# Performance work log

Measured on AMD Instinct MI355X. Metric: run time of the kernel, lower is better.

The kernel has to match this reference:

```python
import jax, jax.numpy as jnp
import numpy as np

NUM_POINTS = 50
PMAX = 4096  # static per-ROI capacity (>> expected max ROI size ~2.2k)
EPS = 1e-5


def _bn(x, g, b):
    # BatchNorm1d in training mode: biased batch variance, eps=1e-5
    m = jnp.mean(x, axis=0)
    v = jnp.var(x, axis=0)
    return g * (x - m) * jax.lax.rsqrt(v + EPS) + b


def _fps(coords, valid, k):
    # coords: [P,3], valid: [P] bool. Classic PointNet++ FPS: start at idx 0,
    # iteratively pick argmax of running min squared distance. Invalid slots
    # pinned to -1 so they are never selected (while any valid point exists).
    dist0 = jnp.where(valid, 1e10, -1.0)

    def step(carry, _):
        dist, last = carry
        d = jnp.sum((coords - coords[last]) ** 2, axis=-1)
        dist = jnp.minimum(dist, jnp.where(valid, d, -1.0))
        nxt = jnp.argmax(dist).astype(jnp.int32)
        return (dist, nxt), nxt

    (_, _), rest = jax.lax.scan(step, (dist0, jnp.int32(0)), None, length=k - 1)
    return jnp.concatenate([jnp.zeros((1,), jnp.int32), rest])


def setup_inputs() -> dict:
    key = jax.random.key(0)
    ks = jax.random.split(key, 16)
    N, R, F, K = 500000, 256, 90, NUM_POINTS
    mid0, mid1, out_dim = 512, 256, 512

    def lin(k, i, o):
        return jax.random.normal(k, (i, o), jnp.float32) * 0.02, jnp.zeros((o,), jnp.float32)

    w1, b1 = lin(ks[0], F * K, mid1)
    w2, b2 = lin(ks[1], mid1, mid1)
    w3, b3 = lin(ks[2], mid1, mid0)
    w4, b4 = lin(ks[3], mid0, mid1)
    w5, b5 = lin(ks[4], mid1, out_dim)
    ones = lambda d: jnp.ones((d,), jnp.float32)
    zeros = lambda d: jnp.zeros((d,), jnp.float32)
    return {
        "cur_roi_nums": R,
        "cur_point_rois_idx": jax.random.randint(ks[5], (N,), 0, R, jnp.int32),
        "cur_points_features": jax.random.normal(ks[6], (N, F), jnp.float32),
        "cur_points_coords": jax.random.normal(ks[7], (N, 3), jnp.float32),
        "w1": w1, "b1": b1, "g1": ones(mid1), "be1": zeros(mid1),
        "w2": w2, "b2": b2, "g2": ones(mid1), "be2": zeros(mid1),
        "w3": w3, "b3": b3, "g3": ones(mid0), "be3": zeros(mid0),
        "w4": w4, "b4": b4, "g4": ones(mid1), "be4": zeros(mid1),
        "w5": w5, "b5": b5, "g5": ones(out_dim), "be5": zeros(out_dim),
    }


def reference(cur_roi_nums, cur_point_rois_idx, cur_points_features, cur_points_coords,
              w1, b1, g1, be1, w2, b2, g2, be2, w3, b3, g3, be3,
              w4, b4, g4, be4, w5, b5, g5, be5):
    R = int(cur_roi_nums)
    N = cur_points_coords.shape[0]
    idx = cur_point_rois_idx
    # Stable sort groups each ROI's points contiguously, preserving point order
    # (same order as the boolean-mask gather in the original loop).
    order = jnp.argsort(idx)
    counts = jnp.bincount(idx, length=R)            # [R]
    offsets = jnp.cumsum(counts) - counts            # [R]
    j = jnp.arange(PMAX)
    pos = offsets[:, None] + j[None, :]              # [R, PMAX]
    valid = j[None, :] < jnp.minimum(counts, PMAX)[:, None]
    gidx = jnp.take(order, jnp.clip(pos, 0, N - 1))  # [R, PMAX] global point ids
    coords_p = jnp.take(cur_points_coords, gidx, axis=0)  # [R, PMAX, 3]

    samp = jax.vmap(lambda c, v: _fps(c, v, NUM_POINTS))(coords_p, valid)  # [R, K]
    sg = jnp.take_along_axis(gidx, samp, axis=1)     # [R, K]
    feat = jnp.take(cur_points_features, sg, axis=0)  # [R, K, 90]
    feat = jnp.where((counts > 0)[:, None, None], feat, 0.0).reshape(R, -1)

    h = jax.nn.relu(_bn(feat @ w1 + b1, g1, be1))
    h = jax.nn.relu(_bn(h @ w2 + b2, g2, be2))
    h = _bn(h @ w3 + b3, g3, be3)
    h = jax.nn.relu(_bn(h @ w4 + b4, g4, be4))
    return jax.nn.relu(_bn(h @ w5 + b5, g5, be5))
```

## Files before the change

kernel.cpp:

```cpp
#include <hip/hip_runtime.h>
#include <cstdint>
#include <cstddef>

#define K_SAMP 50
#define CAP    4096
#define NFEAT  90
#define RROI   256
#define MROWS  256
#define CHUNK  1024
#define FROW   (K_SAMP * NFEAT)

__global__ __launch_bounds__(256) void hist_kernel(
    const int* __restrict__ idx, int* __restrict__ H, int* __restrict__ counts,
    int N, int nC)
{
    __shared__ int h[RROI];
    const int c = blockIdx.x, tid = threadIdx.x;
    h[tid] = 0;
    __syncthreads();
    int p0 = c * CHUNK + tid * 4;
    if (p0 + 3 < N) {
        int4 v = *reinterpret_cast<const int4*>(idx + p0);
        atomicAdd(&h[v.x], 1); atomicAdd(&h[v.y], 1);
        atomicAdd(&h[v.z], 1); atomicAdd(&h[v.w], 1);
    } else {
        #pragma unroll
        for (int j = 0; j < 4; j++)
            if (p0 + j < N) atomicAdd(&h[idx[p0 + j]], 1);
    }
    __syncthreads();
    int v = h[tid];
    H[tid * nC + c] = v;
    if (v) atomicAdd(&counts[tid], v);
}

__device__ __forceinline__ int block_scan256(int v, int& total, int* s_w, int tid)
{
    const int lane = tid & 63, w = tid >> 6;
    int inc = v;
    #pragma unroll
    for (int d = 1; d < 64; d <<= 1) {
        int o = __shfl_up(inc, (unsigned)d);
        if (lane >= d) inc += o;
    }
    if (lane == 63) s_w[w] = inc;
    __syncthreads();
    int woff = 0;
    #pragma unroll
    for (int j = 0; j < 4; j++) woff += (j < w) ? s_w[j] : 0;
    total = s_w[0] + s_w[1] + s_w[2] + s_w[3];
    __syncthreads();
    return woff + inc - v;
}

__global__ __launch_bounds__(256) void chunk_scan_kernel(
    int* __restrict__ H, const int* __restrict__ counts, int* __restrict__ offs, int nC)
{
    __shared__ int s_w[4];
    __shared__ int s_scan[RROI];
    const int r = blockIdx.x, tid = threadIdx.x;
    int tot;
    int e = block_scan256(counts[tid], tot, s_w, tid);
    s_scan[tid] = e;
    __syncthreads();
    const int off = s_scan[r];
    int v0 = (tid < nC) ? H[r * nC + tid] : 0;
    int t0;
    int e0 = block_scan256(v0, t0, s_w, tid);
    if (tid < nC) H[r * nC + tid] = off + e0;
    int c2 = 256 + tid;
    int v1 = (c2 < nC) ? H[r * nC + c2] : 0;
    int t1;
    int e1 = block_scan256(v1, t1, s_w, tid);
    if (c2 < nC) H[r * nC + c2] = off + t0 + e1;
    if (tid == 0) offs[r] = off;
}

__global__ __launch_bounds__(256) void scatter_kernel(
    const int* __restrict__ idx, const float* __restrict__ coords,
    const int* __restrict__ H, int* __restrict__ sGid,
    float* __restrict__ sXc, float* __restrict__ sYc, float* __restrict__ sZc,
    int N, int nC)
{
    __shared__ int s_base[RROI];
    const int c = blockIdx.x, tid = threadIdx.x;
    const int lane = tid & 63, wid = tid >> 6;
    s_base[tid] = H[tid * nC + c];
    int roiA[4]; float cxA[4], cyA[4], czA[4]; bool valA[4];
    #pragma unroll
    for (int j = 0; j < 4; j++) {
        int p = c * CHUNK + j * 256 + tid;
        bool v = p < N;
        valA[j] = v;
        roiA[j] = v ? idx[p] : 0;
        float x = 0.f, y = 0.f, z = 0.f;
        if (v) { x = coords[(size_t)p*3]; y = coords[(size_t)p*3+1]; z = coords[(size_t)p*3+2]; }
        cxA[j] = x; cyA[j] = y; czA[j] = z;
    }
    __syncthreads();
    #pragma unroll
    for (int j = 0; j < 4; j++) {
        #pragma unroll
        for (int w = 0; w < 4; w++) {
            if (wid == w) {
                bool v = valA[j];
                int roi = roiA[j];
                unsigned long long vm = __ballot(v);
                unsigned long long match = vm;
                #pragma unroll
                for (int b = 0; b < 8; b++) {
                    unsigned long long vote = __ballot((roi >> b) & 1);
                    match &= ((roi >> b) & 1) ? vote : ~vote;
                }
                int leader = match ? (__ffsll(match) - 1) : 0;
                int gsz  = (int)__popcll(match);
                int rank = (int)__popcll(match & ((1ull << lane) - 1ull));
                int basev = 0;
                if (match && lane == leader) {
                    basev = s_base[roi];
                    s_base[roi] = basev + gsz;
                }
                basev = __shfl(basev, leader);
                if (v) {
                    int dest = basev + rank;
                    int p = c * CHUNK + j * 256 + tid;
                    sGid[dest] = p;
                    sXc[dest] = cxA[j]; sYc[dest] = cyA[j]; sZc[dest] = czA[j];
                }
            }
            __syncthreads();
        }
    }
}

__global__ __launch_bounds__(512) void fps_feat_kernel(
    const int* __restrict__ offs, const int* __restrict__ counts,
    const float* __restrict__ sXc, const float* __restrict__ sYc,
    const float* __restrict__ sZc, const int* __restrict__ sGid,
    const float* __restrict__ feats, float* __restrict__ feat_out)
{
    __shared__ float sx[CAP], sy[CAP], sz[CAP];
    __shared__ int   sg[CAP];
    __shared__ int   s_samp[K_SAMP];
    __shared__ float s_rv[8];
    __shared__ int   s_ri[8];
    __shared__ int   s_last;

    const int r = blockIdx.x, tid = threadIdx.x;
    const int lane = tid & 63, wid = tid >> 6;
    const int off = offs[r];
    int count = counts[r]; if (count > CAP) count = CAP;

    float rx[8], ry[8], rz[8], rd[8];
    #pragma unroll
    for (int j = 0; j < 8; j++) {
        int i = j * 512 + tid;
        bool v = i < count;
        float x = 0.f, y = 0.f, z = 0.f;
        if (v) {
            x = sXc[off + i]; y = sYc[off + i]; z = sZc[off + i];
            sg[i] = sGid[off + i];
        }
        rx[j] = x; ry[j] = y; rz[j] = z;
        rd[j] = v ? 1e10f : -1.0f;
        sx[i] = x; sy[i] = y; sz[i] = z;
    }
    if (tid == 0) { s_samp[0] = 0; s_last = 0; }
    __syncthreads();

    if (count > 0) {
        int last = 0;
        for (int k = 1; k < K_SAMP; k++) {
            float lx = sx[last], ly = sy[last], lz = sz[last];
            float bv = -3.0e38f; int bi = 0x7fffffff;
            #pragma unroll
            for (int j = 0; j < 8; j++) {
                float dx = rx[j] - lx, dy = ry[j] - ly, dz = rz[j] - lz;
                float d = __fadd_rn(__fadd_rn(__fmul_rn(dx,dx), __fmul_rn(dy,dy)),
                                    __fmul_rn(dz,dz));
                float nd = fminf(rd[j], d);
                rd[j] = nd;
                int i = j * 512 + tid;
                if (nd > bv || (nd == bv && i < bi)) { bv = nd; bi = i; }
            }
            #pragma unroll
            for (int m = 32; m > 0; m >>= 1) {
                float ov = __shfl_xor(bv, m);
                int   oi = __shfl_xor(bi, m);
                if (ov > bv || (ov == bv && oi < bi)) { bv = ov; bi = oi; }
            }
            if (lane == 0) { s_rv[wid] = bv; s_ri[wid] = bi; }
            __syncthreads();
            if (tid == 0) {
                #pragma unroll
                for (int j = 1; j < 8; j++)
                    if (s_rv[j] > bv || (s_rv[j] == bv && s_ri[j] < bi)) {
                        bv = s_rv[j]; bi = s_ri[j];
                    }
                s_samp[k] = bi; s_last = bi;
            }
            __syncthreads();
            last = s_last;
        }
    }
    __syncthreads();

    for (int t = tid; t < FROW; t += 512) {
        int s = t / NFEAT;
        int f = t - s * NFEAT;
        float v = 0.f;
        if (count > 0) {
            int gid = sg[s_samp[s]];
            v = feats[(size_t)gid * NFEAT + f];
        }
        feat_out[(size_t)r * FROW + t] = v;
    }
}

__global__ __launch_bounds__(256) void gemm_splitk(
    const float* __restrict__ A, const float* __restrict__ B, float* __restrict__ C,
    int M, int N, int Kdim, int kc)
{
    __shared__ float As[16][64];
    __shared__ float Bs[16][64];
    const int tid = threadIdx.x;
    const int bm  = blockIdx.y * 64;
    const int bn  = blockIdx.x * 64;
    const int k0  = blockIdx.z * kc;
    const int k1  = (k0 + kc < Kdim) ? (k0 + kc) : Kdim;
    const int ty  = tid >> 4, tx = tid & 15;
    const int am  = tid >> 2, ak = (tid & 3) * 4;
    const int bk  = tid >> 6, bnn = tid & 63;

    float acc[4][4] = {};
    for (int k = k0; k < k1; k += 16) {
        int arow = bm + am;
        float4 av;
        if (k + ak + 3 < Kdim) {
            av = *reinterpret_cast<const float4*>(A + (size_t)arow * Kdim + k + ak);
        } else {
            av.x = (k+ak+0 < Kdim) ? A[(size_t)arow*Kdim + k+ak+0] : 0.f;
            av.y = (k+ak+1 < Kdim) ? A[(size_t)arow*Kdim + k+ak+1] : 0.f;
            av.z = (k+ak+2 < Kdim) ? A[(size_t)arow*Kdim + k+ak+2] : 0.f;
            av.w = (k+ak+3 < Kdim) ? A[(size_t)arow*Kdim + k+ak+3] : 0.f;
        }
        As[ak+0][am] = av.x; As[ak+1][am] = av.y;
        As[ak+2][am] = av.z; As[ak+3][am] = av.w;
        #pragma unroll
        for (int j = 0; j < 4; j++) {
            int kr = bk + j * 4;
            Bs[kr][bnn] = (k + kr < Kdim) ? B[(size_t)(k + kr) * N + bn + bnn] : 0.f;
        }
        __syncthreads();
        #pragma unroll
        for (int kk = 0; kk < 16; kk++) {
            float4 aq = *reinterpret_cast<const float4*>(&As[kk][ty * 4]);
            float4 bq = *reinterpret_cast<const float4*>(&Bs[kk][tx * 4]);
            float a[4] = {aq.x, aq.y, aq.z, aq.w};
            float b[4] = {bq.x, bq.y, bq.z, bq.w};
            #pragma unroll
            for (int i = 0; i < 4; i++)
                #pragma unroll
                for (int j = 0; j < 4; j++)
                    acc[i][j] = fmaf(a[i], b[j], acc[i][j]);
        }
        __syncthreads();
    }
    #pragma unroll
    for (int i = 0; i < 4; i++)
        #pragma unroll
        for (int j = 0; j < 4; j++)
            atomicAdd(&C[(size_t)(bm + ty*4 + i) * N + (bn + tx*4 + j)], acc[i][j]);
}

__global__ __launch_bounds__(256) void bn_kernel(
    const float* __restrict__ X, float* __restrict__ Y,
    const float* __restrict__ g, const float* __restrict__ be, int C, int relu)
{
    const int c = blockIdx.x, t = threadIdx.x;
    const int lane = t & 63, w = t >> 6;
    __shared__ float sw[4], sq[4];

    float x = X[(size_t)t * C + c];
    float s = x;
    #pragma unroll
    for (int d = 32; d > 0; d >>= 1) s += __shfl_xor(s, d);
    if (lane == 0) sw[w] = s;
    __syncthreads();
    float m = (sw[0] + sw[1] + sw[2] + sw[3]) * (1.f / MROWS);
    float dv = x - m;
    float q = dv * dv;
    #pragma unroll
    for (int d = 32; d > 0; d >>= 1) q += __shfl_xor(q, d);
    if (lane == 0) sq[w] = q;
    __syncthreads();
    float v = (sq[0] + sq[1] + sq[2] + sq[3]) * (1.f / MROWS);
    float y = g[c] * dv * rsqrtf(v + 1e-5f) + be[c];
    if (relu) y = fmaxf(y, 0.f);
    Y[(size_t)t * C + c] = y;
}

extern "C" void kernel_launch(void* const* d_in, const int* in_sizes, int n_in,
                              void* d_out, int out_size, void* d_ws, size_t ws_size,
                              hipStream_t stream)
{
    (void)n_in; (void)out_size; (void)ws_size;
    const int*   idx    = (const int*)  d_in[1];
    const float* feats  = (const float*)d_in[2];
    const float* coords = (const float*)d_in[3];
    const float* w1 = (const float*)d_in[4];
    const float* g1 = (const float*)d_in[6];  const float* be1 = (const float*)d_in[7];
    const float* w2 = (const float*)d_in[8];
    const float* g2 = (const float*)d_in[10]; const float* be2 = (const float*)d_in[11];
    const float* w3 = (const float*)d_in[12];
    const float* g3 = (const float*)d_in[14]; const float* be3 = (const float*)d_in[15];
    const float* w4 = (const float*)d_in[16];
    const float* g4 = (const float*)d_in[18]; const float* be4 = (const float*)d_in[19];
    const float* w5 = (const float*)d_in[20];
    const float* g5 = (const float*)d_in[22]; const float* be5 = (const float*)d_in[23];
    const int N  = in_sizes[1];
    const int nC = (N + CHUNK - 1) / CHUNK;

    float* ws   = (float*)d_ws;
    float* feat = ws;
    float* x1   = ws + 1152000;
    float* y1   = x1 + 65536;
    float* x2   = y1 + 65536;
    float* y2   = x2 + 65536;
    float* x3   = y2 + 65536;
    float* y3   = x3 + 131072;
    float* x4   = y3 + 131072;
    float* y4   = x4 + 65536;
    float* x5   = y4 + 65536;
    int*   counts = (int*)(x5 + 131072);
    int*   offs   = counts + 256;
    int*   H      = offs + 256;
    int*   sGid   = H + 256 * 1024;
    float* sXc    = (float*)(sGid + N);
    float* sYc    = sXc + N;
    float* sZc    = sYc + N;
    float* out    = (float*)d_out;

    hipMemsetAsync(x1, 0, (size_t)(786432 + 256) * sizeof(float), stream);

    hist_kernel      <<<nC,  256, 0, stream>>>(idx, H, counts, N, nC);
    chunk_scan_kernel<<<256, 256, 0, stream>>>(H, counts, offs, nC);
    scatter_kernel   <<<nC,  256, 0, stream>>>(idx, coords, H, sGid, sXc, sYc, sZc, N, nC);
    fps_feat_kernel  <<<256, 512, 0, stream>>>(offs, counts, sXc, sYc, sZc, sGid, feats, feat);

    gemm_splitk<<<dim3(4,4,16), 256, 0, stream>>>(feat, w1, x1, 256, 256, 4500, 288);
    bn_kernel  <<<256, 256, 0, stream>>>(x1, y1, g1, be1, 256, 1);
    gemm_splitk<<<dim3(4,4,2), 256, 0, stream>>>(y1, w2, x2, 256, 256, 256, 128);
    bn_kernel  <<<256, 256, 0, stream>>>(x2, y2, g2, be2, 256, 1);
    gemm_splitk<<<dim3(8,4,2), 256, 0, stream>>>(y2, w3, x3, 256, 512, 256, 128);
    bn_kernel  <<<512, 256, 0, stream>>>(x3, y3, g3, be3, 512, 0);
    gemm_splitk<<<dim3(4,4,4), 256, 0, stream>>>(y3, w4, x4, 256, 256, 512, 128);
    bn_kernel  <<<256, 256, 0, stream>>>(x4, y4, g4, be4, 256, 1);
    gemm_splitk<<<dim3(8,4,2), 256, 0, stream>>>(y4, w5, x5, 256, 512, 256, 128);
    bn_kernel  <<<512, 256, 0, stream>>>(x5, out, g5, be5, 512, 1);
}
```

Baseline: 560.0 us.

## Fuse MLP GEMM and batchnorm stages into one persistent kernel with grid barriers

```diff
diff --git a/kernel.cpp b/kernel.cpp
--- a/kernel.cpp
+++ b/kernel.cpp
@@ -9,6 +9,7 @@
 #define MROWS  256
 #define CHUNK  1024
 #define FROW   (K_SAMP * NFEAT)
+#define NB     256
 
 __global__ __launch_bounds__(256) void hist_kernel(
     const int* __restrict__ idx, int* __restrict__ H, int* __restrict__ counts,
@@ -217,20 +218,37 @@
     }
 }
 
-__global__ __launch_bounds__(256) void gemm_splitk(
+__device__ __forceinline__ void gbar(int* bar, int target)
+{
+    __syncthreads();
+    if (threadIdx.x == 0) {
+        __threadfence();
+        __hip_atomic_fetch_add(bar, 1, __ATOMIC_ACQ_REL, __HIP_MEMORY_SCOPE_AGENT);
+        while (__hip_atomic_load(bar, __ATOMIC_ACQUIRE, __HIP_MEMORY_SCOPE_AGENT) < target)
+            __builtin_amdgcn_s_sleep(2);
+        __threadfence();
+    }
+    __syncthreads();
+}
+
+__device__ __forceinline__ void gemm_phase(
     const float* __restrict__ A, const float* __restrict__ B, float* __restrict__ C,
-    int M, int N, int Kdim, int kc)
-{
-    __shared__ float As[16][64];
-    __shared__ float Bs[16][64];
+    int Ncols, int Kdim, int gx, int gy, int gz, int kc,
+    float (*As)[64], float (*Bs)[64])
+{
+    const int vb = blockIdx.x;
+    if (vb >= gx * gy * gz) return;
     const int tid = threadIdx.x;
-    const int bm  = blockIdx.y * 64;
-    const int bn  = blockIdx.x * 64;
-    const int k0  = blockIdx.z * kc;
-    const int k1  = (k0 + kc < Kdim) ? (k0 + kc) : Kdim;
-    const int ty  = tid >> 4, tx = tid & 15;
-    const int am  = tid >> 2, ak = (tid & 3) * 4;
-    const int bk  = tid >> 6, bnn = tid & 63;
+    const int bx = vb % gx;
+    const int by = (vb / gx) % gy;
+    const int bz = vb / (gx * gy);
+    const int bm = by * 64;
+    const int bn = bx * 64;
+    const int k0 = bz * kc;
+    const int k1 = (k0 + kc < Kdim) ? (k0 + kc) : Kdim;
+    const int ty = tid >> 4, tx = tid & 15;
+    const int am = tid >> 2, ak = (tid & 3) * 4;
+    const int bk = tid >> 6, bnn = tid & 63;
 
     float acc[4][4] = {};
     for (int k = k0; k < k1; k += 16) {
@@ -249,7 +267,7 @@
         #pragma unroll
         for (int j = 0; j < 4; j++) {
             int kr = bk + j * 4;
-            Bs[kr][bnn] = (k + kr < Kdim) ? B[(size_t)(k + kr) * N + bn + bnn] : 0.f;
+            Bs[kr][bnn] = (k + kr < Kdim) ? B[(size_t)(k + kr) * Ncols + bn + bnn] : 0.f;
         }
         __syncthreads();
         #pragma unroll
@@ -270,34 +288,69 @@
     for (int i = 0; i < 4; i++)
         #pragma unroll
         for (int j = 0; j < 4; j++)
-            atomicAdd(&C[(size_t)(bm + ty*4 + i) * N + (bn + tx*4 + j)], acc[i][j]);
-}
-
-__global__ __launch_bounds__(256) void bn_kernel(
+            atomicAdd(&C[(size_t)(bm + ty*4 + i) * Ncols + (bn + tx*4 + j)], acc[i][j]);
+}
+
+__device__ __forceinline__ void bn_phase(
     const float* __restrict__ X, float* __restrict__ Y,
-    const float* __restrict__ g, const float* __restrict__ be, int C, int relu)
-{
-    const int c = blockIdx.x, t = threadIdx.x;
-    const int lane = t & 63, w = t >> 6;
-    __shared__ float sw[4], sq[4];
-
-    float x = X[(size_t)t * C + c];
-    float s = x;
-    #pragma unroll
-    for (int d = 32; d > 0; d >>= 1) s += __shfl_xor(s, d);
-    if (lane == 0) sw[w] = s;
-    __syncthreads();
-    float m = (sw[0] + sw[1] + sw[2] + sw[3]) * (1.f / MROWS);
-    float dv = x - m;
-    float q = dv * dv;
-    #pragma unroll
-    for (int d = 32; d > 0; d >>= 1) q += __shfl_xor(q, d);
-    if (lane == 0) sq[w] = q;
-    __syncthreads();
-    float v = (sq[0] + sq[1] + sq[2] + sq[3]) * (1.f / MROWS);
-    float y = g[c] * dv * rsqrtf(v + 1e-5f) + be[c];
-    if (relu) y = fmaxf(y, 0.f);
-    Y[(size_t)t * C + c] = y;
+    const float* __restrict__ g, const float* __restrict__ be,
+    int C, int relu, float* sred)
+{
+    const int t = threadIdx.x, lane = t & 63, w = t >> 6;
+    for (int c = blockIdx.x; c < C; c += NB) {
+        float x = X[(size_t)t * C + c];
+        float s = x;
+        #pragma unroll
+        for (int d = 32; d > 0; d >>= 1) s += __shfl_xor(s, d);
+        if (lane == 0) sred[w] = s;
+        __syncthreads();
+        float m = (sred[0] + sred[1] + sred[2] + sred[3]) * (1.f / MROWS);
+        float dv = x - m;
+        float q = dv * dv;
+        #pragma unroll
+        for (int d = 32; d > 0; d >>= 1) q += __shfl_xor(q, d);
+        if (lane == 0) sred[4 + w] = q;
+        __syncthreads();
+        float v = (sred[4] + sred[5] + sred[6] + sred[7]) * (1.f / MROWS);
+        float y = g[c] * dv * rsqrtf(v + 1e-5f) + be[c];
+        if (relu) y = fmaxf(y, 0.f);
+        Y[(size_t)t * C + c] = y;
+        __syncthreads();
+    }
+}
+
+__global__ __launch_bounds__(256) void mlp_fused_kernel(
+    const float* __restrict__ feat,
+    const float* __restrict__ w1, const float* __restrict__ g1, const float* __restrict__ be1,
+    const float* __restrict__ w2, const float* __restrict__ g2, const float* __restrict__ be2,
+    const float* __restrict__ w3, const float* __restrict__ g3, const float* __restrict__ be3,
+    const float* __restrict__ w4, const float* __restrict__ g4, const float* __restrict__ be4,
+    const float* __restrict__ w5, const float* __restrict__ g5, const float* __restrict__ be5,
+    float* __restrict__ x1, float* __restrict__ x2, float* __restrict__ x3,
+    float* __restrict__ x4, float* __restrict__ x5, float* __restrict__ out,
+    int* bar)
+{
+    __shared__ float As[16][64];
+    __shared__ float Bs[16][64];
+    __shared__ float sred[8];
+
+    {
+        float4* z = reinterpret_cast<float4*>(x1);
+        const int nz = 458752 / 4;
+        for (int i = blockIdx.x * 256 + threadIdx.x; i < nz; i += NB * 256)
+            z[i] = float4{0.f, 0.f, 0.f, 0.f};
+    }
+    gbar(bar, 1 * NB);
+    gemm_phase(feat, w1, x1, 256, 4500, 4, 4, 16, 288, As, Bs);  gbar(bar, 2 * NB);
+    bn_phase(x1, x1, g1, be1, 256, 1, sred);                     gbar(bar, 3 * NB);
+    gemm_phase(x1, w2, x2, 256, 256, 4, 4, 4, 64, As, Bs);       gbar(bar, 4 * NB);
+    bn_phase(x2, x2, g2, be2, 256, 1, sred);                     gbar(bar, 5 * NB);
+    gemm_phase(x2, w3, x3, 512, 256, 8, 4, 4, 64, As, Bs);       gbar(bar, 6 * NB);
+    bn_phase(x3, x3, g3, be3, 512, 0, sred);                     gbar(bar, 7 * NB);
+    gemm_phase(x3, w4, x4, 256, 512, 4, 4, 8, 64, As, Bs);       gbar(bar, 8 * NB);
+    bn_phase(x4, x4, g4, be4, 256, 1, sred);                     gbar(bar, 9 * NB);
+    gemm_phase(x4, w5, x5, 512, 256, 8, 4, 4, 64, As, Bs);       gbar(bar, 10 * NB);
+    bn_phase(x5, out, g5, be5, 512, 1, sred);
 }
 
 extern "C" void kernel_launch(void* const* d_in, const int* in_sizes, int n_in,
@@ -324,16 +377,13 @@
     float* ws   = (float*)d_ws;
     float* feat = ws;
     float* x1   = ws + 1152000;
-    float* y1   = x1 + 65536;
-    float* x2   = y1 + 65536;
-    float* y2   = x2 + 65536;
-    float* x3   = y2 + 65536;
-    float* y3   = x3 + 131072;
-    float* x4   = y3 + 131072;
-    float* y4   = x4 + 65536;
-    float* x5   = y4 + 65536;
+    float* x2   = x1 + 65536;
+    float* x3   = x2 + 65536;
+    float* x4   = x3 + 131072;
+    float* x5   = x4 + 65536;
     int*   counts = (int*)(x5 + 131072);
-    int*   offs   = counts + 256;
+    int*   bar    = counts + 256;
+    int*   offs   = bar + 16;
     int*   H      = offs + 256;
     int*   sGid   = H + 256 * 1024;
     float* sXc    = (float*)(sGid + N);
@@ -341,21 +391,14 @@
     float* sZc    = sYc + N;
     float* out    = (float*)d_out;
 
-    hipMemsetAsync(x1, 0, (size_t)(786432 + 256) * sizeof(float), stream);
+    hipMemsetAsync(counts, 0, 272 * sizeof(int), stream);
 
     hist_kernel      <<<nC,  256, 0, stream>>>(idx, H, counts, N, nC);
     chunk_scan_kernel<<<256, 256, 0, stream>>>(H, counts, offs, nC);
     scatter_kernel   <<<nC,  256, 0, stream>>>(idx, coords, H, sGid, sXc, sYc, sZc, N, nC);
     fps_feat_kernel  <<<256, 512, 0, stream>>>(offs, counts, sXc, sYc, sZc, sGid, feats, feat);
 
-    gemm_splitk<<<dim3(4,4,16), 256, 0, stream>>>(feat, w1, x1, 256, 256, 4500, 288);
-    bn_kernel  <<<256, 256, 0, stream>>>(x1, y1, g1, be1, 256, 1);
-    gemm_splitk<<<dim3(4,4,2), 256, 0, stream>>>(y1, w2, x2, 256, 256, 256, 128);
-    bn_kernel  <<<256, 256, 0, stream>>>(x2, y2, g2, be2, 256, 1);
-    gemm_splitk<<<dim3(8,4,2), 256, 0, stream>>>(y2, w3, x3, 256, 512, 256, 128);
-    bn_kernel  <<<512, 256, 0, stream>>>(x3, y3, g3, be3, 512, 0);
-    gemm_splitk<<<dim3(4,4,4), 256, 0, stream>>>(y3, w4, x4, 256, 256, 512, 128);
-    bn_kernel  <<<256, 256, 0, stream>>>(x4, y4, g4, be4, 256, 1);
-    gemm_splitk<<<dim3(8,4,2), 256, 0, stream>>>(y4, w5, x5, 256, 512, 256, 128);
-    bn_kernel  <<<512, 256, 0, stream>>>(x5, out, g5, be5, 512, 1);
-}
+    mlp_fused_kernel <<<NB, 256, 0, stream>>>(
+        feat, w1, g1, be1, w2, g2, be2, w3, g3, be3, w4, g4, be4, w5, g5, be5,
+        x1, x2, x3, x4, x5, out, bar);
+}
```

Measured after the change: 846.7 us. 51.2% more time.

## Fuse MLP GEMMs with BatchNorm and replace atomic split-K with partial buffers

Applied to the files above, without the earlier changes.

```diff
diff --git a/kernel.cpp b/kernel.cpp
--- a/kernel.cpp
+++ b/kernel.cpp
@@ -217,9 +217,9 @@
     }
 }
 
-__global__ __launch_bounds__(256) void gemm_splitk(
-    const float* __restrict__ A, const float* __restrict__ B, float* __restrict__ C,
-    int M, int N, int Kdim, int kc)
+__global__ __launch_bounds__(256) void gemm1_splitk_kernel(
+    const float* __restrict__ A, const float* __restrict__ B, float* __restrict__ P,
+    int Kdim, int kc)
 {
     __shared__ float As[16][64];
     __shared__ float Bs[16][64];
@@ -249,7 +249,7 @@
         #pragma unroll
         for (int j = 0; j < 4; j++) {
             int kr = bk + j * 4;
-            Bs[kr][bnn] = (k + kr < Kdim) ? B[(size_t)(k + kr) * N + bn + bnn] : 0.f;
+            Bs[kr][bnn] = (k + kr < Kdim) ? B[(size_t)(k + kr) * 256 + bn + bnn] : 0.f;
         }
         __syncthreads();
         #pragma unroll
@@ -266,38 +266,113 @@
         }
         __syncthreads();
     }
-    #pragma unroll
-    for (int i = 0; i < 4; i++)
-        #pragma unroll
-        for (int j = 0; j < 4; j++)
-            atomicAdd(&C[(size_t)(bm + ty*4 + i) * N + (bn + tx*4 + j)], acc[i][j]);
-}
-
-__global__ __launch_bounds__(256) void bn_kernel(
-    const float* __restrict__ X, float* __restrict__ Y,
-    const float* __restrict__ g, const float* __restrict__ be, int C, int relu)
-{
-    const int c = blockIdx.x, t = threadIdx.x;
-    const int lane = t & 63, w = t >> 6;
-    __shared__ float sw[4], sq[4];
-
-    float x = X[(size_t)t * C + c];
-    float s = x;
-    #pragma unroll
-    for (int d = 32; d > 0; d >>= 1) s += __shfl_xor(s, d);
-    if (lane == 0) sw[w] = s;
-    __syncthreads();
-    float m = (sw[0] + sw[1] + sw[2] + sw[3]) * (1.f / MROWS);
-    float dv = x - m;
-    float q = dv * dv;
-    #pragma unroll
-    for (int d = 32; d > 0; d >>= 1) q += __shfl_xor(q, d);
-    if (lane == 0) sq[w] = q;
-    __syncthreads();
-    float v = (sq[0] + sq[1] + sq[2] + sq[3]) * (1.f / MROWS);
-    float y = g[c] * dv * rsqrtf(v + 1e-5f) + be[c];
-    if (relu) y = fmaxf(y, 0.f);
-    Y[(size_t)t * C + c] = y;
+    float* Pz = P + (size_t)blockIdx.z * 65536;
+    #pragma unroll
+    for (int i = 0; i < 4; i++) {
+        float4 o = {acc[i][0], acc[i][1], acc[i][2], acc[i][3]};
+        *reinterpret_cast<float4*>(&Pz[(size_t)(bm + ty*4 + i) * 256 + bn + tx*4]) = o;
+    }
+}
+
+__device__ __forceinline__ void bn_store(
+    float (&acc)[32], const float* __restrict__ g, const float* __restrict__ be,
+    float* __restrict__ Y, int NC, int bn, int relu,
+    float (*red)[64], int lane, int w)
+{
+    float s = 0.f;
+    #pragma unroll
+    for (int i = 0; i < 32; i++) s += acc[i];
+    red[w][lane] = s;
+    __syncthreads();
+    float m = 0.f;
+    #pragma unroll
+    for (int j = 0; j < 8; j++) m += red[j][lane];
+    m *= (1.f / 256.f);
+    float q = 0.f;
+    #pragma unroll
+    for (int i = 0; i < 32; i++) { float d = acc[i] - m; q += d * d; }
+    __syncthreads();
+    red[w][lane] = q;
+    __syncthreads();
+    float v = 0.f;
+    #pragma unroll
+    for (int j = 0; j < 8; j++) v += red[j][lane];
+    v *= (1.f / 256.f);
+    float sc = g[bn + lane] * rsqrtf(v + 1e-5f);
+    float bi = be[bn + lane];
+    #pragma unroll
+    for (int i = 0; i < 32; i++) {
+        float y = (acc[i] - m) * sc + bi;
+        if (relu) y = fmaxf(y, 0.f);
+        Y[(size_t)(w * 32 + i) * NC + bn + lane] = y;
+    }
+}
+
+__global__ __launch_bounds__(512) void sum_bn_kernel(
+    const float* __restrict__ P, const float* __restrict__ g,
+    const float* __restrict__ be, float* __restrict__ Y)
+{
+    __shared__ float red[8][64];
+    const int tid = threadIdx.x, lane = tid & 63, w = tid >> 6;
+    const int bn = blockIdx.x * 64;
+    float acc[32];
+    #pragma unroll
+    for (int i = 0; i < 32; i++) acc[i] = 0.f;
+    for (int z = 0; z < 16; z++) {
+        const float* Pz = P + (size_t)z * 65536;
+        #pragma unroll
+        for (int i = 0; i < 32; i++)
+            acc[i] += Pz[(size_t)(w * 32 + i) * 256 + bn + lane];
+    }
+    bn_store(acc, g, be, Y, 256, bn, 1, red, lane, w);
+}
+
+template<int KD, int NC, int RELU>
+__global__ __launch_bounds__(512) void gemm_bn_kernel(
+    const float* __restrict__ A, const float* __restrict__ B,
+    const float* __restrict__ g, const float* __restrict__ be,
+    float* __restrict__ Y)
+{
+    __shared__ float As[16][260];
+    __shared__ float Bs[16][64];
+    __shared__ float red[8][64];
+    const int tid  = threadIdx.x;
+    const int lane = tid & 63;
+    const int w    = tid >> 6;
+    const int bn   = blockIdx.x * 64;
+    const int r    = tid >> 1;
+    const int hf   = (tid & 1) * 8;
+    const int bkk  = tid >> 5;
+    const int bc   = (tid & 31) * 2;
+
+    float acc[32];
+    #pragma unroll
+    for (int i = 0; i < 32; i++) acc[i] = 0.f;
+
+    for (int k0 = 0; k0 < KD; k0 += 16) {
+        float4 a0 = *reinterpret_cast<const float4*>(A + (size_t)r * KD + k0 + hf);
+        float4 a1 = *reinterpret_cast<const float4*>(A + (size_t)r * KD + k0 + hf + 4);
+        float2 bv = *reinterpret_cast<const float2*>(B + (size_t)(k0 + bkk) * NC + bn + bc);
+        __syncthreads();
+        As[hf+0][r] = a0.x; As[hf+1][r] = a0.y; As[hf+2][r] = a0.z; As[hf+3][r] = a0.w;
+        As[hf+4][r] = a1.x; As[hf+5][r] = a1.y; As[hf+6][r] = a1.z; As[hf+7][r] = a1.w;
+        Bs[bkk][bc] = bv.x; Bs[bkk][bc+1] = bv.y;
+        __syncthreads();
+        #pragma unroll
+        for (int kk = 0; kk < 16; kk++) {
+            float b = Bs[kk][lane];
+            #pragma unroll
+            for (int i2 = 0; i2 < 8; i2++) {
+                float4 a = *reinterpret_cast<const float4*>(&As[kk][w * 32 + i2 * 4]);
+                acc[i2*4+0] = fmaf(a.x, b, acc[i2*4+0]);
+                acc[i2*4+1] = fmaf(a.y, b, acc[i2*4+1]);
+                acc[i2*4+2] = fmaf(a.z, b, acc[i2*4+2]);
+                acc[i2*4+3] = fmaf(a.w, b, acc[i2*4+3]);
+            }
+        }
+    }
+    __syncthreads();
+    bn_store(acc, g, be, Y, NC, bn, RELU, red, lane, w);
 }
 
 extern "C" void kernel_launch(void* const* d_in, const int* in_sizes, int n_in,
@@ -323,16 +398,12 @@
 
     float* ws   = (float*)d_ws;
     float* feat = ws;
-    float* x1   = ws + 1152000;
-    float* y1   = x1 + 65536;
-    float* x2   = y1 + 65536;
-    float* y2   = x2 + 65536;
-    float* x3   = y2 + 65536;
-    float* y3   = x3 + 131072;
-    float* x4   = y3 + 131072;
-    float* y4   = x4 + 65536;
-    float* x5   = y4 + 65536;
-    int*   counts = (int*)(x5 + 131072);
+    float* P    = ws + 1152000;
+    float* y1   = P + 1048576;
+    float* y2   = y1 + 65536;
+    float* y3   = y2 + 65536;
+    float* y4   = y3 + 131072;
+    int*   counts = (int*)(y4 + 65536);
     int*   offs   = counts + 256;
     int*   H      = offs + 256;
     int*   sGid   = H + 256 * 1024;
@@ -341,21 +412,17 @@
     float* sZc    = sYc + N;
     float* out    = (float*)d_out;
 
-    hipMemsetAsync(x1, 0, (size_t)(786432 + 256) * sizeof(float), stream);
+    hipMemsetAsync(counts, 0, 256 * sizeof(int), stream);
 
     hist_kernel      <<<nC,  256, 0, stream>>>(idx, H, counts, N, nC);
     chunk_scan_kernel<<<256, 256, 0, stream>>>(H, counts, offs, nC);
     scatter_kernel   <<<nC,  256, 0, stream>>>(idx, coords, H, sGid, sXc, sYc, sZc, N, nC);
     fps_feat_kernel  <<<256, 512, 0, stream>>>(offs, counts, sXc, sYc, sZc, sGid, feats, feat);
 
-    gemm_splitk<<<dim3(4,4,16), 256, 0, stream>>>(feat, w1, x1, 256, 256, 4500, 288);
-    bn_kernel  <<<256, 256, 0, stream>>>(x1, y1, g1, be1, 256, 1);
-    gemm_splitk<<<dim3(4,4,2), 256, 0, stream>>>(y1, w2, x2, 256, 256, 256, 128);
-    bn_kernel  <<<256, 256, 0, stream>>>(x2, y2, g2, be2, 256, 1);
-    gemm_splitk<<<dim3(8,4,2), 256, 0, stream>>>(y2, w3, x3, 256, 512, 256, 128);
-    bn_kernel  <<<512, 256, 0, stream>>>(x3, y3, g3, be3, 512, 0);
-    gemm_splitk<<<dim3(4,4,4), 256, 0, stream>>>(y3, w4, x4, 256, 256, 512, 128);
-    bn_kernel  <<<256, 256, 0, stream>>>(x4, y4, g4, be4, 256, 1);
-    gemm_splitk<<<dim3(8,4,2), 256, 0, stream>>>(y4, w5, x5, 256, 512, 256, 128);
-    bn_kernel  <<<512, 256, 0, stream>>>(x5, out, g5, be5, 512, 1);
-}
+    gemm1_splitk_kernel<<<dim3(4,4,16), 256, 0, stream>>>(feat, w1, P, 4500, 288);
+    sum_bn_kernel      <<<4, 512, 0, stream>>>(P, g1, be1, y1);
+    gemm_bn_kernel<256,256,1><<<4, 512, 0, stream>>>(y1, w2, g2, be2, y2);
+    gemm_bn_kernel<256,512,0><<<8, 512, 0, stream>>>(y2, w3, g3, be3, y3);
+    gemm_bn_kernel<512,256,1><<<4, 512, 0, stream>>>(y3, w4, g4, be4, y4);
+    gemm_bn_kernel<256,512,1><<<8, 512, 0, stream>>>(y4, w5, g5, be5, out);
+}
```

Result: slower. 663.2 us (+18.4%).
